# Performance work log

Hardware: AMD Instinct MI355X
Metric: run time of the kernel (lower is better)

The kernel has to match this reference:

```python
import jax, jax.numpy as jnp
import numpy as np

D_IN = 1024
D_OUT = 1024
NUM_HEADS = 16
HEAD_DIM = D_OUT // NUM_HEADS
SCALE = HEAD_DIM ** -0.5


def setup_inputs() -> dict:
    key = jax.random.key(0)
    k_x, k_qkv, k_pw, k_pb = jax.random.split(key, 4)
    B, S = 2, 2048
    x = jax.random.normal(k_x, (B, S, D_IN), dtype=jnp.float32)
    # nn.Linear weights: stored as (out_features, in_features); qkv_bias=False
    w_qkv = jax.random.normal(k_qkv, (3 * D_OUT, D_IN), dtype=jnp.float32) * (D_IN ** -0.5)
    w_proj = jax.random.normal(k_pw, (D_OUT, D_OUT), dtype=jnp.float32) * (D_OUT ** -0.5)
    b_proj = jax.random.normal(k_pb, (D_OUT,), dtype=jnp.float32) * 0.01
    return {"x": x, "w_qkv": w_qkv, "w_proj": w_proj, "b_proj": b_proj}


def reference(x, w_qkv, w_proj, b_proj):
    B, S, _ = x.shape
    # combined QKV projection: (B,S,3*d_out)
    qkv = jnp.einsum('bsd,ed->bse', x, w_qkv)
    qkv = qkv.reshape(B, S, 3, NUM_HEADS, HEAD_DIM)
    qkv = jnp.transpose(qkv, (2, 0, 3, 1, 4))  # (3,B,H,S,hd)
    q, k, v = qkv[0], qkv[1], qkv[2]
    scores = jnp.einsum('bhqd,bhkd->bhqk', q, k)  # (B,H,S,S)
    causal = jnp.triu(jnp.ones((S, S), dtype=bool), k=1)
    # module masks to -inf first, then scales (softmax-equivalent)
    scores = jnp.where(causal, -jnp.inf, scores) * SCALE
    attn = jax.nn.softmax(scores, axis=-1)
    ctx = jnp.einsum('bhqk,bhkd->bhqd', attn, v)
    ctx = jnp.transpose(ctx, (0, 2, 1, 3)).reshape(B, S, D_OUT)
    return jnp.einsum('bsd,ed->bse', ctx, w_proj) + b_proj
```

## Files before the change

kernel.cpp:

```cpp
#include <hip/hip_runtime.h>

#define SEQ    2048
#define NHEAD  16
#define HDIM   64
#define DMODEL 1024
#define BATCH  2

typedef __bf16 bf16;
typedef __bf16 bf16x8 __attribute__((ext_vector_type(8)));
typedef __bf16 bf16x4v __attribute__((ext_vector_type(4)));
typedef float  f32x4  __attribute__((ext_vector_type(4)));

typedef const __attribute__((address_space(1))) void* gas_ptr;
typedef __attribute__((address_space(3))) void*       las_ptr;

__device__ __forceinline__ f32x4 mfma16(bf16x8 a, bf16x8 b, f32x4 c) {
  return __builtin_amdgcn_mfma_f32_16x16x32_bf16(a, b, c, 0, 0, 0);
}

__device__ __forceinline__ void gload_lds16(const void* g, void* l) {
  __builtin_amdgcn_global_load_lds((gas_ptr)(unsigned long long)g,
                                   (las_ptr)(unsigned long long)l, 16, 0, 0);
}

__global__ void convert_all(const float* __restrict__ x, const float* __restrict__ wq,
                            const float* __restrict__ wp, bf16* __restrict__ out) {
  const long long NX = 4194304, NQ = 3145728, NP = 1048576;
  long long i = ((long long)blockIdx.x * blockDim.x + threadIdx.x) * 4;
  if (i >= NX + NQ + NP) return;
  const float* src; long long off;
  if (i < NX)           { src = x;  off = i; }
  else if (i < NX + NQ) { src = wq; off = i - NX; }
  else                  { src = wp; off = i - NX - NQ; }
  float4 f = *reinterpret_cast<const float4*>(src + off);
  bf16x4v r;
  r[0] = (bf16)f.x; r[1] = (bf16)f.y; r[2] = (bf16)f.z; r[3] = (bf16)f.w;
  *reinterpret_cast<bf16x4v*>(out + i) = r;
}

template <int EPI>
__global__ __launch_bounds__(256) void gemm_bt(
    const bf16* __restrict__ A, const bf16* __restrict__ B, int K,
    bf16* __restrict__ q, bf16* __restrict__ k, bf16* __restrict__ v,
    const float* __restrict__ bias, float* __restrict__ out) {
  __shared__ alignas(16) bf16 As[2][128 * 32];
  __shared__ alignas(16) bf16 Bs[2][128 * 32];

  const int tid = threadIdx.x;
  const int l = tid & 63, w = tid >> 6;
  const int lr = l & 15, lg = l >> 4;
  const int wr = (w >> 1) * 64, wc = (w & 1) * 64;
  const long long m0 = (long long)blockIdx.x * 128;
  const long long n0 = (long long)blockIdx.y * 128;
  const int crow = tid >> 2, ccol = (tid & 3) * 8;

  auto stage = [&](int kt, int buf) {
    const bf16* a_src = A + (m0 + crow) * K + (long long)kt * 32 + ccol;
    const bf16* b_src = B + (n0 + crow) * K + (long long)kt * 32 + ccol;
    gload_lds16(a_src,           &As[buf][tid * 8]);
    gload_lds16(a_src + 64LL * K, &As[buf][(tid + 256) * 8]);
    gload_lds16(b_src,           &Bs[buf][tid * 8]);
    gload_lds16(b_src + 64LL * K, &Bs[buf][(tid + 256) * 8]);
  };

  f32x4 acc[4][4];
  const f32x4 fz = {0.f, 0.f, 0.f, 0.f};
#pragma unroll
  for (int m = 0; m < 4; ++m)
#pragma unroll
    for (int n = 0; n < 4; ++n) acc[m][n] = fz;

  stage(0, 0);
  const int nk = K >> 5;
  int cur = 0;
  for (int kt = 0; kt < nk; ++kt) {
    __syncthreads();
    if (kt + 1 < nk) stage(kt + 1, cur ^ 1);
    bf16x8 af[4], bfv[4];
#pragma unroll
    for (int m = 0; m < 4; ++m)
      af[m] = *reinterpret_cast<const bf16x8*>(&As[cur][(wr + m * 16 + lr) * 32 + lg * 8]);
#pragma unroll
    for (int n = 0; n < 4; ++n)
      bfv[n] = *reinterpret_cast<const bf16x8*>(&Bs[cur][(wc + n * 16 + lr) * 32 + lg * 8]);
#pragma unroll
    for (int m = 0; m < 4; ++m)
#pragma unroll
      for (int n = 0; n < 4; ++n) acc[m][n] = mfma16(af[m], bfv[n], acc[m][n]);
    cur ^= 1;
  }

#pragma unroll
  for (int m = 0; m < 4; ++m) {
#pragma unroll
    for (int n = 0; n < 4; ++n) {
#pragma unroll
      for (int j = 0; j < 4; ++j) {
        long long grow = m0 + wr + m * 16 + lg * 4 + j;
        long long gcol = n0 + wc + n * 16 + lr;
        float val = acc[m][n][j];
        if (EPI == 0) {
          int three = (int)(gcol >> 10);
          int rem = (int)(gcol & 1023);
          int h = rem >> 6, d = rem & 63;
          int b = (int)(grow >> 11), s = (int)(grow & 2047);
          int bh = b * NHEAD + h;
          if (three < 2) {
            int dst = ((bh * 128 + (s >> 4)) * 2 + (d >> 5)) * 512 +
                      (s & 15) * 32 + ((d >> 3) & 3) * 8 + (d & 7);
            if (three == 0) q[dst] = (bf16)(val * 0.125f);
            else            k[dst] = (bf16)val;
          } else {
            int dst = (((bh * 4 + (d >> 4)) * 32 + (s >> 6)) * 2 + ((s >> 5) & 1)) * 512 +
                      (d & 15) * 32 + ((s >> 3) & 3) * 8 + (s & 7);
            v[dst] = (bf16)val;
          }
        } else {
          out[grow * 1024 + gcol] = val + bias[gcol];
        }
      }
    }
  }
}

__global__ __launch_bounds__(256, 2) void attn_kernel(
    const bf16* __restrict__ qbuf, const bf16* __restrict__ kbuf,
    const bf16* __restrict__ vbuf, bf16* __restrict__ ctx) {
  const int lid = blockIdx.y * gridDim.x + blockIdx.x;
  const int xcd = lid & 7;
  const int idx = lid >> 3;
  const int bh  = xcd + (idx >> 4) * 8;
  const int p   = idx & 15;
  const int tid = threadIdx.x;
  const int l = tid & 63, w = tid >> 6;
  const int lr = l & 15, lg = l >> 4;
  const int foff = lr * 32 + lg * 8;

  __shared__ alignas(16) bf16 Pl[4][16][72];

  const bf16* Kb = kbuf + bh * 131072 + foff;
  const bf16* Vb = vbuf + bh * 131072 + foff;
  const int b = bh >> 4, h = bh & 15;
  const f32x4 fz = {0.f, 0.f, 0.f, 0.f};

  f32x4 o[4];
  float mrow[4], lsum[4];
  bf16x8 qf[2];

  bf16x8 kA[4][2], vA[4][2], kB[4][2], vB[4][2];

#pragma unroll
  for (int nd = 0; nd < 4; ++nd)
#pragma unroll
    for (int kk = 0; kk < 2; ++kk) {
      vA[nd][kk] = *reinterpret_cast<const bf16x8*>(&Vb[((nd * 32 + 0) * 2 + kk) * 512]);
      kA[nd][kk] = *reinterpret_cast<const bf16x8*>(&Kb[((0 * 4 + nd) * 2 + kk) * 512]);
    }

  auto step = [&](bf16x8 (&kc)[4][2], bf16x8 (&vc)[4][2],
                  bf16x8 (&kn)[4][2], bf16x8 (&vn)[4][2], int i) {
    const bool in_a = (i <= p);
    const int qt = in_a ? p : 31 - p;
    const int kt = in_a ? i : i - p - 1;
    const bool diag = (kt == qt);

    if (kt == 0) {
      const int qt16 = qt * 4 + w;
      const bf16* Qb = qbuf + (bh * 128 + qt16) * 1024 + foff;
      qf[0] = *reinterpret_cast<const bf16x8*>(Qb);
      qf[1] = *reinterpret_cast<const bf16x8*>(Qb + 512);
#pragma unroll
      for (int nd = 0; nd < 4; ++nd) o[nd] = fz;
#pragma unroll
      for (int j = 0; j < 4; ++j) { mrow[j] = -1e30f; lsum[j] = 0.f; }
    }

    {
      const int i2 = i + 1;
      int kt2 = (i2 <= p) ? i2 : i2 - p - 1;
      if (i2 > 32) kt2 = 0;
#pragma unroll
      for (int nd = 0; nd < 4; ++nd)
#pragma unroll
        for (int kk = 0; kk < 2; ++kk) {
          vn[nd][kk] = *reinterpret_cast<const bf16x8*>(&Vb[((nd * 32 + kt2) * 2 + kk) * 512]);
          kn[nd][kk] = *reinterpret_cast<const bf16x8*>(&Kb[((kt2 * 4 + nd) * 2 + kk) * 512]);
        }
    }

    f32x4 s4[4];
#pragma unroll
    for (int n = 0; n < 4; ++n)
      s4[n] = mfma16(qf[1], kc[n][1], mfma16(qf[0], kc[n][0], fz));
    if (diag) {
#pragma unroll
      for (int n = 0; n < 4; ++n)
#pragma unroll
        for (int j = 0; j < 4; ++j)
          if (n * 16 + lr > w * 16 + lg * 4 + j) s4[n][j] = -1e30f;
    }

    float pm[4];
#pragma unroll
    for (int j = 0; j < 4; ++j)
      pm[j] = fmaxf(fmaxf(s4[0][j], s4[1][j]), fmaxf(s4[2][j], s4[3][j]));
#pragma unroll
    for (int msk = 1; msk <= 8; msk <<= 1)
#pragma unroll
      for (int j = 0; j < 4; ++j) pm[j] = fmaxf(pm[j], __shfl_xor(pm[j], msk, 64));
    float alpha[4];
#pragma unroll
    for (int j = 0; j < 4; ++j) {
      float mn = fmaxf(mrow[j], pm[j]);
      alpha[j] = __expf(mrow[j] - mn);
      mrow[j] = mn;
    }
    float rs[4] = {0.f, 0.f, 0.f, 0.f};
#pragma unroll
    for (int n = 0; n < 4; ++n)
#pragma unroll
      for (int j = 0; j < 4; ++j) {
        float pv = __expf(s4[n][j] - mrow[j]);
        s4[n][j] = pv;
        rs[j] += pv;
      }
#pragma unroll
    for (int j = 0; j < 4; ++j) lsum[j] = lsum[j] * alpha[j] + rs[j];
#pragma unroll
    for (int nd = 0; nd < 4; ++nd)
#pragma unroll
      for (int j = 0; j < 4; ++j) o[nd][j] *= alpha[j];

#pragma unroll
    for (int n = 0; n < 4; ++n)
#pragma unroll
      for (int j = 0; j < 4; ++j)
        Pl[w][lg * 4 + j][n * 16 + lr] = (bf16)s4[n][j];

#pragma unroll
    for (int kk = 0; kk < 2; ++kk) {
      bf16x8 pf = *reinterpret_cast<const bf16x8*>(&Pl[w][lr][kk * 32 + lg * 8]);
#pragma unroll
      for (int nd = 0; nd < 4; ++nd)
        o[nd] = mfma16(pf, vc[nd][kk], o[nd]);
    }

    if (diag) {
      float ls[4];
#pragma unroll
      for (int j = 0; j < 4; ++j) ls[j] = lsum[j];
#pragma unroll
      for (int msk = 1; msk <= 8; msk <<= 1)
#pragma unroll
        for (int j = 0; j < 4; ++j) ls[j] += __shfl_xor(ls[j], msk, 64);
      float inv[4];
#pragma unroll
      for (int j = 0; j < 4; ++j) inv[j] = 1.0f / ls[j];
      const int qr0 = (qt * 4 + w) * 16;
#pragma unroll
      for (int nd = 0; nd < 4; ++nd)
#pragma unroll
        for (int j = 0; j < 4; ++j) {
          int srow = qr0 + lg * 4 + j;
          int d = nd * 16 + lr;
          ctx[((long long)(b * SEQ + srow)) * DMODEL + h * HDIM + d] =
              (bf16)(o[nd][j] * inv[j]);
        }
    }
  };

  for (int i = 0; i < 33; i += 2) {
    step(kA, vA, kB, vB, i);
    if (i + 1 < 33) step(kB, vB, kA, vA, i + 1);
  }
}

extern "C" void kernel_launch(void* const* d_in, const int* in_sizes, int n_in,
                              void* d_out, int out_size, void* d_ws, size_t ws_size,
                              hipStream_t stream) {
  const float* x      = (const float*)d_in[0];
  const float* w_qkv  = (const float*)d_in[1];
  const float* w_proj = (const float*)d_in[2];
  const float* b_proj = (const float*)d_in[3];
  float* out = (float*)d_out;

  bf16* ws = (bf16*)d_ws;
  bf16* xb     = ws;
  bf16* wqkvb  = xb + 4194304;
  bf16* wprojb = wqkvb + 3145728;
  bf16* qb     = wprojb + 1048576;
  bf16* kb     = qb + 4194304;
  bf16* vb     = kb + 4194304;
  bf16* ctxb   = vb + 4194304;

  convert_all<<<8192, 256, 0, stream>>>(x, w_qkv, w_proj, xb);
  gemm_bt<0><<<dim3(32, 24), 256, 0, stream>>>(xb, wqkvb, 1024, qb, kb, vb, nullptr, nullptr);
  attn_kernel<<<dim3(16, 32), 256, 0, stream>>>(qb, kb, vb, ctxb);
  gemm_bt<1><<<dim3(32, 8), 256, 0, stream>>>(ctxb, wprojb, 1024, nullptr, nullptr, nullptr,
                                              b_proj, out);
}
```

Measured before the change: 200.5 us.

## Stage K/V tiles in shared LDS via async loads and defer softmax rescaling

```diff
diff --git a/kernel.cpp b/kernel.cpp
--- a/kernel.cpp
+++ b/kernel.cpp
@@ -107,12 +107,12 @@
           int bh = b * NHEAD + h;
           if (three < 2) {
             int dst = ((bh * 128 + (s >> 4)) * 2 + (d >> 5)) * 512 +
-                      (s & 15) * 32 + ((d >> 3) & 3) * 8 + (d & 7);
-            if (three == 0) q[dst] = (bf16)(val * 0.125f);
+                      (s & 15) * 8 + ((d >> 3) & 3) * 128 + (d & 7);
+            if (three == 0) q[dst] = (bf16)(val * 0.18033688f);
             else            k[dst] = (bf16)val;
           } else {
             int dst = (((bh * 4 + (d >> 4)) * 32 + (s >> 6)) * 2 + ((s >> 5) & 1)) * 512 +
-                      (d & 15) * 32 + ((s >> 3) & 3) * 8 + (s & 7);
+                      (d & 15) * 8 + ((s >> 3) & 3) * 128 + (s & 7);
             v[dst] = (bf16)val;
           }
         } else {
@@ -134,64 +134,62 @@
   const int tid = threadIdx.x;
   const int l = tid & 63, w = tid >> 6;
   const int lr = l & 15, lg = l >> 4;
-  const int foff = lr * 32 + lg * 8;
-
+  const int loff = l * 8;
+
+  __shared__ alignas(16) bf16 Ks[2][4096];
+  __shared__ alignas(16) bf16 Vs[2][4096];
   __shared__ alignas(16) bf16 Pl[4][16][72];
 
-  const bf16* Kb = kbuf + bh * 131072 + foff;
-  const bf16* Vb = vbuf + bh * 131072 + foff;
+  const bf16* Kg = kbuf + bh * 131072;
+  const bf16* Vg = vbuf + bh * 131072;
   const int b = bh >> 4, h = bh & 15;
   const f32x4 fz = {0.f, 0.f, 0.f, 0.f};
+
+  auto stage = [&](int kt, int sb) {
+#pragma unroll
+    for (int j = 0; j < 2; ++j) {
+      const int c = 2 * w + j;
+      gload_lds16(Kg + kt * 4096 + c * 512 + loff, &Ks[sb][c * 512 + loff]);
+      gload_lds16(Vg + w * 32768 + kt * 1024 + j * 512 + loff, &Vs[sb][c * 512 + loff]);
+    }
+  };
 
   f32x4 o[4];
   float mrow[4], lsum[4];
   bf16x8 qf[2];
 
-  bf16x8 kA[4][2], vA[4][2], kB[4][2], vB[4][2];
-
-#pragma unroll
-  for (int nd = 0; nd < 4; ++nd)
-#pragma unroll
-    for (int kk = 0; kk < 2; ++kk) {
-      vA[nd][kk] = *reinterpret_cast<const bf16x8*>(&Vb[((nd * 32 + 0) * 2 + kk) * 512]);
-      kA[nd][kk] = *reinterpret_cast<const bf16x8*>(&Kb[((0 * 4 + nd) * 2 + kk) * 512]);
-    }
-
-  auto step = [&](bf16x8 (&kc)[4][2], bf16x8 (&vc)[4][2],
-                  bf16x8 (&kn)[4][2], bf16x8 (&vn)[4][2], int i) {
+  stage(0, 0);
+  __syncthreads();
+  int buf = 0;
+
+  for (int i = 0; i < 33; ++i) {
     const bool in_a = (i <= p);
     const int qt = in_a ? p : 31 - p;
     const int kt = in_a ? i : i - p - 1;
     const bool diag = (kt == qt);
 
     if (kt == 0) {
-      const int qt16 = qt * 4 + w;
-      const bf16* Qb = qbuf + (bh * 128 + qt16) * 1024 + foff;
-      qf[0] = *reinterpret_cast<const bf16x8*>(Qb);
-      qf[1] = *reinterpret_cast<const bf16x8*>(Qb + 512);
+      const bf16* Qb = qbuf + (bh * 128 + qt * 4 + w) * 1024;
+      qf[0] = *reinterpret_cast<const bf16x8*>(Qb + loff);
+      qf[1] = *reinterpret_cast<const bf16x8*>(Qb + 512 + loff);
 #pragma unroll
       for (int nd = 0; nd < 4; ++nd) o[nd] = fz;
 #pragma unroll
       for (int j = 0; j < 4; ++j) { mrow[j] = -1e30f; lsum[j] = 0.f; }
     }
 
-    {
+    if (i + 1 < 33) {
       const int i2 = i + 1;
-      int kt2 = (i2 <= p) ? i2 : i2 - p - 1;
-      if (i2 > 32) kt2 = 0;
-#pragma unroll
-      for (int nd = 0; nd < 4; ++nd)
-#pragma unroll
-        for (int kk = 0; kk < 2; ++kk) {
-          vn[nd][kk] = *reinterpret_cast<const bf16x8*>(&Vb[((nd * 32 + kt2) * 2 + kk) * 512]);
-          kn[nd][kk] = *reinterpret_cast<const bf16x8*>(&Kb[((kt2 * 4 + nd) * 2 + kk) * 512]);
-        }
+      stage((i2 <= p) ? i2 : i2 - p - 1, buf ^ 1);
     }
 
     f32x4 s4[4];
 #pragma unroll
-    for (int n = 0; n < 4; ++n)
-      s4[n] = mfma16(qf[1], kc[n][1], mfma16(qf[0], kc[n][0], fz));
+    for (int n = 0; n < 4; ++n) {
+      bf16x8 k0 = *reinterpret_cast<const bf16x8*>(&Ks[buf][(n * 2 + 0) * 512 + loff]);
+      bf16x8 k1 = *reinterpret_cast<const bf16x8*>(&Ks[buf][(n * 2 + 1) * 512 + loff]);
+      s4[n] = mfma16(qf[1], k1, mfma16(qf[0], k0, fz));
+    }
     if (diag) {
 #pragma unroll
       for (int n = 0; n < 4; ++n)
@@ -201,35 +199,39 @@
     }
 
     float pm[4];
-#pragma unroll
-    for (int j = 0; j < 4; ++j)
+    float dmax = -1e30f;
+#pragma unroll
+    for (int j = 0; j < 4; ++j) {
       pm[j] = fmaxf(fmaxf(s4[0][j], s4[1][j]), fmaxf(s4[2][j], s4[3][j]));
-#pragma unroll
-    for (int msk = 1; msk <= 8; msk <<= 1)
-#pragma unroll
-      for (int j = 0; j < 4; ++j) pm[j] = fmaxf(pm[j], __shfl_xor(pm[j], msk, 64));
-    float alpha[4];
-#pragma unroll
-    for (int j = 0; j < 4; ++j) {
-      float mn = fmaxf(mrow[j], pm[j]);
-      alpha[j] = __expf(mrow[j] - mn);
-      mrow[j] = mn;
-    }
+      dmax = fmaxf(dmax, pm[j] - mrow[j]);
+    }
+    if (__any(dmax > 11.0f)) {
+#pragma unroll
+      for (int msk = 1; msk <= 8; msk <<= 1)
+#pragma unroll
+        for (int j = 0; j < 4; ++j) pm[j] = fmaxf(pm[j], __shfl_xor(pm[j], msk, 64));
+#pragma unroll
+      for (int j = 0; j < 4; ++j) {
+        float mn = fmaxf(mrow[j], pm[j]);
+        float alpha = exp2f(mrow[j] - mn);
+        mrow[j] = mn;
+        lsum[j] *= alpha;
+#pragma unroll
+        for (int nd = 0; nd < 4; ++nd) o[nd][j] *= alpha;
+      }
+    }
+
     float rs[4] = {0.f, 0.f, 0.f, 0.f};
 #pragma unroll
     for (int n = 0; n < 4; ++n)
 #pragma unroll
       for (int j = 0; j < 4; ++j) {
-        float pv = __expf(s4[n][j] - mrow[j]);
+        float pv = exp2f(s4[n][j] - mrow[j]);
         s4[n][j] = pv;
         rs[j] += pv;
       }
 #pragma unroll
-    for (int j = 0; j < 4; ++j) lsum[j] = lsum[j] * alpha[j] + rs[j];
-#pragma unroll
-    for (int nd = 0; nd < 4; ++nd)
-#pragma unroll
-      for (int j = 0; j < 4; ++j) o[nd][j] *= alpha[j];
+    for (int j = 0; j < 4; ++j) lsum[j] += rs[j];
 
 #pragma unroll
     for (int n = 0; n < 4; ++n)
@@ -241,8 +243,10 @@
     for (int kk = 0; kk < 2; ++kk) {
       bf16x8 pf = *reinterpret_cast<const bf16x8*>(&Pl[w][lr][kk * 32 + lg * 8]);
 #pragma unroll
-      for (int nd = 0; nd < 4; ++nd)
-        o[nd] = mfma16(pf, vc[nd][kk], o[nd]);
+      for (int nd = 0; nd < 4; ++nd) {
+        bf16x8 vfr = *reinterpret_cast<const bf16x8*>(&Vs[buf][(nd * 2 + kk) * 512 + loff]);
+        o[nd] = mfma16(pf, vfr, o[nd]);
+      }
     }
 
     if (diag) {
@@ -267,11 +271,9 @@
               (bf16)(o[nd][j] * inv[j]);
         }
     }
-  };
-
-  for (int i = 0; i < 33; i += 2) {
-    step(kA, vA, kB, vB, i);
-    if (i + 1 < 33) step(kB, vB, kA, vA, i + 1);
+
+    __syncthreads();
+    buf ^= 1;
   }
 }
 
```

Result: faster. 186.8 us (-6.8%).
